# Kernel tuning notes

Measured on AMD Instinct MI355X. Metric: run time of the kernel, lower is better.

## Reference

```python
import jax, jax.numpy as jnp
import numpy as np

N_NODES = 50000
N_EDGES = 800000
FIN = 128
FQK = 128
FV = 128
H = 8


def setup_inputs() -> dict:
    key = jax.random.key(0)
    k1, k2, k3, k4, k5 = jax.random.split(key, 5)
    x = jax.random.normal(k1, (N_NODES, FIN), dtype=jnp.float32)
    # nn.Linear(Fin, 2*Fqk+Fv, bias=False): weight shape [Ftot, Fin]
    W = jax.random.normal(k2, (2 * FQK + FV, FIN), dtype=jnp.float32) / np.sqrt(FIN)
    # src must be sorted (scatter_* assume batch[-1]+1 segments)
    src = jnp.sort(jax.random.randint(k3, (N_EDGES,), 0, N_NODES))
    dest = jax.random.randint(k4, (N_EDGES,), 0, N_NODES)
    ei = jnp.stack([src, dest])
    batch = jnp.sort(jax.random.randint(k5, (N_NODES,), 0, 64))
    return {"x": x, "W": W, "batch": batch, "ei": ei}


def reference(x, W, batch, ei):
    n = x.shape[0]
    Fh = FQK // H    # 16
    Fhv = FV // H    # 16
    scaling = float(Fh) ** (-0.5)
    src, dest = ei[0], ei[1]

    qkv = x @ W.T                                   # [n, 2*Fqk+Fv]
    q = (qkv[:, :FQK] * scaling).reshape(n, H, Fh)
    k = qkv[:, FQK:2 * FQK].reshape(n, H, Fh)
    v = qkv[:, 2 * FQK:].reshape(n, H, Fhv)

    # per-edge attention scores, one per head: [E, H]
    aw = jnp.einsum('ehf,ehf->eh', q[src], k[dest])
    # faithful to original scatter_softmax: subtract GLOBAL per-head max
    aw = aw - aw.max(axis=0)
    ex = jnp.exp(aw)
    denom = jax.ops.segment_sum(ex, src, num_segments=n)[src]   # [E, H]
    a = ex / denom

    out = jax.ops.segment_sum(a[:, :, None] * v[dest], src, num_segments=n)  # [n, H, Fhv]
    return out.reshape(n, H * Fhv)
```

## Files before the change

kernel.cpp:

```cpp
#include <hip/hip_runtime.h>
#include <hip/hip_fp16.h>
#include <math.h>

#define FIN_ 128

typedef _Float16 half2v __attribute__((ext_vector_type(2)));
typedef _Float16 half8v __attribute__((ext_vector_type(8)));
typedef __attribute__((ext_vector_type(4))) float float4v;

__device__ __forceinline__ half2v u2h(unsigned u) {
    union { unsigned u; half2v h; } c; c.u = u; return c.h;
}

__device__ __forceinline__ half8v cvt8(float4 a, float4 b) {
    half8v r;
    r[0] = (_Float16)a.x; r[1] = (_Float16)a.y;
    r[2] = (_Float16)a.z; r[3] = (_Float16)a.w;
    r[4] = (_Float16)b.x; r[5] = (_Float16)b.y;
    r[6] = (_Float16)b.z; r[7] = (_Float16)b.w;
    return r;
}

__global__ __launch_bounds__(256) void gemm_qkv_mfma(const float* __restrict__ x,
                                                     const float* __restrict__ W,
                                                     _Float16* __restrict__ qb,
                                                     _Float16* __restrict__ kv,
                                                     int n) {
    __shared__ _Float16 smem[2 * 128 * 68];
    _Float16 (*xs)[68] = (_Float16(*)[68])smem;
    _Float16 (*ws)[68] = (_Float16(*)[68])(smem + 128 * 68);
    const int row0 = blockIdx.x * 128;
    const int f0   = blockIdx.y * 128;
    const int t = threadIdx.x;
    const int lane = t & 63;
    const int wave = t >> 6;
    const int wr = wave >> 1, wc = wave & 1;
    const int l15 = lane & 15, kg = lane >> 4;

    float4v acc[4][4];
#pragma unroll
    for (int i = 0; i < 4; ++i)
#pragma unroll
        for (int j = 0; j < 4; ++j) acc[i][j] = (float4v)0.f;

    const int r5 = t >> 3;
    const int c8 = (t & 7) * 8;

    for (int half = 0; half < 2; ++half) {
        __syncthreads();
#pragma unroll
        for (int p = 0; p < 4; ++p) {
            const int row = p * 32 + r5;
            const int gxr = row0 + row;
            float4 u0 = make_float4(0.f, 0.f, 0.f, 0.f), u1 = u0;
            if (gxr < n) {
                u0 = *(const float4*)&x[(size_t)gxr * FIN_ + half * 64 + c8];
                u1 = *(const float4*)&x[(size_t)gxr * FIN_ + half * 64 + c8 + 4];
            }
            *(half8v*)&xs[row][c8] = cvt8(u0, u1);
            const float4 w0 = *(const float4*)&W[(size_t)(f0 + row) * FIN_ + half * 64 + c8];
            const float4 w1 = *(const float4*)&W[(size_t)(f0 + row) * FIN_ + half * 64 + c8 + 4];
            *(half8v*)&ws[row][c8] = cvt8(w0, w1);
        }
        __syncthreads();
#pragma unroll
        for (int ks = 0; ks < 2; ++ks) {
            const int kcol = ks * 32 + kg * 8;
            half8v a[4], b[4];
#pragma unroll
            for (int mi = 0; mi < 4; ++mi)
                a[mi] = *(half8v*)&ws[wr * 64 + mi * 16 + l15][kcol];
#pragma unroll
            for (int ni = 0; ni < 4; ++ni)
                b[ni] = *(half8v*)&xs[wc * 64 + ni * 16 + l15][kcol];
#pragma unroll
            for (int mi = 0; mi < 4; ++mi)
#pragma unroll
                for (int ni = 0; ni < 4; ++ni)
                    acc[mi][ni] = __builtin_amdgcn_mfma_f32_16x16x32_f16(
                        a[mi], b[ni], acc[mi][ni], 0, 0, 0);
        }
    }

    __syncthreads();
    _Float16 (*T)[136] = (_Float16(*)[136])smem;
    const bool isq = (f0 == 0);
    const float s = isq ? 0.25f : 1.0f;
#pragma unroll
    for (int mi = 0; mi < 4; ++mi) {
        const int fb = wr * 64 + mi * 16 + kg * 4;
#pragma unroll
        for (int ni = 0; ni < 4; ++ni) {
            const int nl = wc * 64 + ni * 16 + l15;
            union { ushort4 u; _Float16 f[4]; } pk;
#pragma unroll
            for (int r = 0; r < 4; ++r) pk.f[r] = (_Float16)(acc[mi][ni][r] * s);
            *(ushort4*)&T[nl][fb] = pk.u;
        }
    }
    __syncthreads();
#pragma unroll
    for (int i = 0; i < 8; ++i) {
        const int u = t + i * 256;
        const int nl = u >> 4;
        const int cs = (u & 15) * 8;
        const int ng = row0 + nl;
        if (ng >= n) continue;
        const half8v val = *(const half8v*)&T[nl][cs];
        if (isq) *(half8v*)&qb[(size_t)ng * 128 + cs] = val;
        else     *(half8v*)&kv[(size_t)ng * 256 + (f0 - 128) + cs] = val;
    }
}

__global__ void build_rowptr(const int* __restrict__ src, int nE,
                             int* __restrict__ rowptr, int n) {
    int i = blockIdx.x * blockDim.x + threadIdx.x;
    if (i > n) return;
    int lo = 0, hi = nE;
    while (lo < hi) {
        int mid = (lo + hi) >> 1;
        if (src[mid] < i) lo = mid + 1; else hi = mid;
    }
    rowptr[i] = lo;
}

__device__ __forceinline__ float dot16(uint4 k0, uint4 k1, const half2v* q) {
#if __has_builtin(__builtin_amdgcn_fdot2)
    float s = __builtin_amdgcn_fdot2(u2h(k0.x), q[0], 0.f, false);
    s = __builtin_amdgcn_fdot2(u2h(k0.y), q[1], s, false);
    s = __builtin_amdgcn_fdot2(u2h(k0.z), q[2], s, false);
    s = __builtin_amdgcn_fdot2(u2h(k0.w), q[3], s, false);
    s = __builtin_amdgcn_fdot2(u2h(k1.x), q[4], s, false);
    s = __builtin_amdgcn_fdot2(u2h(k1.y), q[5], s, false);
    s = __builtin_amdgcn_fdot2(u2h(k1.z), q[6], s, false);
    s = __builtin_amdgcn_fdot2(u2h(k1.w), q[7], s, false);
    return s;
#else
    half2v a = u2h(k0.x) * q[0];
    a += u2h(k0.y) * q[1];
    a += u2h(k0.z) * q[2];
    a += u2h(k0.w) * q[3];
    a += u2h(k1.x) * q[4];
    a += u2h(k1.y) * q[5];
    a += u2h(k1.z) * q[6];
    a += u2h(k1.w) * q[7];
    return (float)a[0] + (float)a[1];
#endif
}

__global__ __launch_bounds__(256) void attn_edges_ep(const _Float16* __restrict__ qb,
                                                     const _Float16* __restrict__ kv,
                                                     const int* __restrict__ rowptr,
                                                     const int* __restrict__ dest,
                                                     float* __restrict__ out, int n) {
    const int wave = threadIdx.x >> 6;
    const int node = blockIdx.x * 4 + wave;
    if (node >= n) return;
    const int lane = threadIdx.x & 63;
    const int j = lane >> 3;
    const int h = lane & 7;
    const int ppos = ((j & 1) << 3) | ((j & 2) << 1) | ((j & 4) >> 1);
    float* outp = &out[(size_t)node * FIN_ + h * 16 + ppos];

    const int e0 = rowptr[node];
    const int e1 = rowptr[node + 1];
    if (e0 == e1) {
        *(float2*)outp = make_float2(0.f, 0.f);
        return;
    }

    half2v qh[8];
    {
        const uint4 q0 = *(const uint4*)(qb + (size_t)node * 128 + h * 16);
        const uint4 q1 = *(const uint4*)(qb + (size_t)node * 128 + h * 16 + 8);
        qh[0] = u2h(q0.x); qh[1] = u2h(q0.y); qh[2] = u2h(q0.z); qh[3] = u2h(q0.w);
        qh[4] = u2h(q1.x); qh[5] = u2h(q1.y); qh[6] = u2h(q1.z); qh[7] = u2h(q1.w);
    }

    float lsum = 0.f;
    half2v a8[8];
#pragma unroll
    for (int i = 0; i < 8; ++i) a8[i] = (half2v)(_Float16)0;

    const int hoff = h << 4;
    for (int eb = e0; eb < e1; eb += 16) {
        const int eA = eb + j;
        const int eB = eb + 8 + j;
        const bool vA = eA < e1;
        const bool vB = eB < e1;
        const unsigned dA = (unsigned)dest[vA ? eA : (e1 - 1)];
        const unsigned dB = (unsigned)dest[vB ? eB : (e1 - 1)];
        const unsigned offA = (dA << 8) + hoff;
        const unsigned offB = (dB << 8) + hoff;
        const uint4 k0A = *(const uint4*)(kv + offA);
        const uint4 k1A = *(const uint4*)(kv + offA + 8);
        const uint4 v0A = *(const uint4*)(kv + offA + 128);
        const uint4 v1A = *(const uint4*)(kv + offA + 136);
        const uint4 k0B = *(const uint4*)(kv + offB);
        const uint4 k1B = *(const uint4*)(kv + offB + 8);
        const uint4 v0B = *(const uint4*)(kv + offB + 128);
        const uint4 v1B = *(const uint4*)(kv + offB + 136);

        const float sA = dot16(k0A, k1A, qh);
        const float sB = dot16(k0B, k1B, qh);
        const float pA = vA ? __expf(sA) : 0.f;
        const float pB = vB ? __expf(sB) : 0.f;
        lsum += pA + pB;

        const _Float16 ha = (_Float16)pA, hb = (_Float16)pB;
        const half2v pa = {ha, ha}, pb = {hb, hb};
        a8[0] += pa * u2h(v0A.x) + pb * u2h(v0B.x);
        a8[1] += pa * u2h(v0A.y) + pb * u2h(v0B.y);
        a8[2] += pa * u2h(v0A.z) + pb * u2h(v0B.z);
        a8[3] += pa * u2h(v0A.w) + pb * u2h(v0B.w);
        a8[4] += pa * u2h(v1A.x) + pb * u2h(v1B.x);
        a8[5] += pa * u2h(v1A.y) + pb * u2h(v1B.y);
        a8[6] += pa * u2h(v1A.z) + pb * u2h(v1B.z);
        a8[7] += pa * u2h(v1A.w) + pb * u2h(v1B.w);
    }

    lsum += __shfl_xor(lsum, 8);
    lsum += __shfl_xor(lsum, 16);
    lsum += __shfl_xor(lsum, 32);

    float a16[16];
#pragma unroll
    for (int i = 0; i < 8; ++i) {
        a16[2 * i]     = (float)a8[i][0];
        a16[2 * i + 1] = (float)a8[i][1];
    }

    float r8[8];
    {
        const bool b = (j & 1) != 0;
#pragma unroll
        for (int i = 0; i < 8; ++i) {
            const float keep = b ? a16[i + 8] : a16[i];
            const float send = b ? a16[i] : a16[i + 8];
            r8[i] = keep + __shfl_xor(send, 8);
        }
    }
    float r4[4];
    {
        const bool b = (j & 2) != 0;
#pragma unroll
        for (int i = 0; i < 4; ++i) {
            const float keep = b ? r8[i + 4] : r8[i];
            const float send = b ? r8[i] : r8[i + 4];
            r4[i] = keep + __shfl_xor(send, 16);
        }
    }
    float r2[2];
    {
        const bool b = (j & 4) != 0;
#pragma unroll
        for (int i = 0; i < 2; ++i) {
            const float keep = b ? r4[i + 2] : r4[i];
            const float send = b ? r4[i] : r4[i + 2];
            r2[i] = keep + __shfl_xor(send, 32);
        }
    }

    const float inv = (lsum > 0.f) ? 1.f / lsum : 0.f;
    *(float2*)outp = make_float2(r2[0] * inv, r2[1] * inv);
}

extern "C" void kernel_launch(void* const* d_in, const int* in_sizes, int n_in,
                              void* d_out, int out_size, void* d_ws, size_t ws_size,
                              hipStream_t stream) {
    const float* x = (const float*)d_in[0];
    const float* W = (const float*)d_in[1];
    const int* ei = (const int*)d_in[3];

    const int n = in_sizes[0] / FIN_;
    const int nE = in_sizes[3] / 2;
    const int* src = ei;
    const int* dest = ei + nE;

    char* w = (char*)d_ws;
    _Float16* qb = (_Float16*)w;   w += (size_t)n * 128 * 2;
    _Float16* kv = (_Float16*)w;   w += (size_t)n * 256 * 2;
    int* rowptr = (int*)w;
    float* out = (float*)d_out;

    build_rowptr<<<(n + 1 + 255) / 256, 256, 0, stream>>>(src, nE, rowptr, n);

    dim3 g1((n + 127) / 128, 3);
    gemm_qkv_mfma<<<g1, 256, 0, stream>>>(x, W, qb, kv, n);

    attn_edges_ep<<<(n + 3) / 4, 256, 0, stream>>>(qb, kv, rowptr, dest, out, n);
}
```

Measured before the change: 99.74 us.

## Fuse rowptr build into QKV GEMM kernel and load MFMA operands directly from global

Merges the rowptr binary-search kernel and the QKV GEMM into one launch, using extra blocks for the rowptr work, which removes a kernel launch and its gap. The GEMM no longer stages x and W through shared memory. Each lane loads and converts its MFMA fragments straight from global memory, so the staging syncs go away at the cost of redundant, less coalesced global reads that rely on L2/L1. The three feature-block tiles for a row block are now adjacent in block order to improve x reuse in cache. The output transpose buffer is halved and written in two phases, which lowers LDS use and may raise occupancy.

```diff
diff --git a/kernel.cpp b/kernel.cpp
--- a/kernel.cpp
+++ b/kernel.cpp
@@ -3,6 +3,7 @@
 #include <math.h>
 
 #define FIN_ 128
+#define NGB_ 3
 
 typedef _Float16 half2v __attribute__((ext_vector_type(2)));
 typedef _Float16 half8v __attribute__((ext_vector_type(8)));
@@ -21,17 +22,32 @@
     return r;
 }
 
-__global__ __launch_bounds__(256) void gemm_qkv_mfma(const float* __restrict__ x,
-                                                     const float* __restrict__ W,
-                                                     _Float16* __restrict__ qb,
-                                                     _Float16* __restrict__ kv,
-                                                     int n) {
-    __shared__ _Float16 smem[2 * 128 * 68];
-    _Float16 (*xs)[68] = (_Float16(*)[68])smem;
-    _Float16 (*ws)[68] = (_Float16(*)[68])(smem + 128 * 68);
-    const int row0 = blockIdx.x * 128;
-    const int f0   = blockIdx.y * 128;
+__global__ __launch_bounds__(256) void prep_kernel(const float* __restrict__ x,
+                                                   const float* __restrict__ W,
+                                                   _Float16* __restrict__ qb,
+                                                   _Float16* __restrict__ kv,
+                                                   const int* __restrict__ src,
+                                                   int* __restrict__ rowptr,
+                                                   int n, int nE, int nxb) {
+    const int bid = blockIdx.x;
     const int t = threadIdx.x;
+
+    if (bid >= 3 * nxb) {
+        const int i = (bid - 3 * nxb) * 256 + t;
+        if (i > n) return;
+        int lo = 0, hi = nE;
+        while (lo < hi) {
+            int mid = (lo + hi) >> 1;
+            if (src[mid] < i) lo = mid + 1; else hi = mid;
+        }
+        rowptr[i] = lo;
+        return;
+    }
+
+    __shared__ _Float16 T[64][136];
+    const int bx = bid / 3, fsel = bid % 3;
+    const int row0 = bx * 128;
+    const int f0 = fsel * 128;
     const int lane = t & 63;
     const int wave = t >> 6;
     const int wr = wave >> 1, wc = wave & 1;
@@ -43,36 +59,30 @@
 #pragma unroll
         for (int j = 0; j < 4; ++j) acc[i][j] = (float4v)0.f;
 
-    const int r5 = t >> 3;
-    const int c8 = (t & 7) * 8;
-
+    int nodeIdx[4];
+#pragma unroll
+    for (int ni = 0; ni < 4; ++ni) {
+        const int nd = row0 + wc * 64 + ni * 16 + l15;
+        nodeIdx[ni] = (nd < n) ? nd : 0;
+    }
+    const size_t fbase = (size_t)(f0 + wr * 64 + l15) * FIN_;
+
+#pragma unroll
     for (int half = 0; half < 2; ++half) {
-        __syncthreads();
-#pragma unroll
-        for (int p = 0; p < 4; ++p) {
-            const int row = p * 32 + r5;
-            const int gxr = row0 + row;
-            float4 u0 = make_float4(0.f, 0.f, 0.f, 0.f), u1 = u0;
-            if (gxr < n) {
-                u0 = *(const float4*)&x[(size_t)gxr * FIN_ + half * 64 + c8];
-                u1 = *(const float4*)&x[(size_t)gxr * FIN_ + half * 64 + c8 + 4];
-            }
-            *(half8v*)&xs[row][c8] = cvt8(u0, u1);
-            const float4 w0 = *(const float4*)&W[(size_t)(f0 + row) * FIN_ + half * 64 + c8];
-            const float4 w1 = *(const float4*)&W[(size_t)(f0 + row) * FIN_ + half * 64 + c8 + 4];
-            *(half8v*)&ws[row][c8] = cvt8(w0, w1);
-        }
-        __syncthreads();
 #pragma unroll
         for (int ks = 0; ks < 2; ++ks) {
-            const int kcol = ks * 32 + kg * 8;
+            const int koff = half * 64 + ks * 32 + kg * 8;
             half8v a[4], b[4];
 #pragma unroll
-            for (int mi = 0; mi < 4; ++mi)
-                a[mi] = *(half8v*)&ws[wr * 64 + mi * 16 + l15][kcol];
-#pragma unroll
-            for (int ni = 0; ni < 4; ++ni)
-                b[ni] = *(half8v*)&xs[wc * 64 + ni * 16 + l15][kcol];
+            for (int mi = 0; mi < 4; ++mi) {
+                const float* p = W + fbase + (size_t)mi * 16 * FIN_ + koff;
+                a[mi] = cvt8(*(const float4*)p, *(const float4*)(p + 4));
+            }
+#pragma unroll
+            for (int ni = 0; ni < 4; ++ni) {
+                const float* p = x + (size_t)nodeIdx[ni] * FIN_ + koff;
+                b[ni] = cvt8(*(const float4*)p, *(const float4*)(p + 4));
+            }
 #pragma unroll
             for (int mi = 0; mi < 4; ++mi)
 #pragma unroll
@@ -82,46 +92,38 @@
         }
     }
 
-    __syncthreads();
-    _Float16 (*T)[136] = (_Float16(*)[136])smem;
-    const bool isq = (f0 == 0);
+    const bool isq = (fsel == 0);
     const float s = isq ? 0.25f : 1.0f;
-#pragma unroll
-    for (int mi = 0; mi < 4; ++mi) {
-        const int fb = wr * 64 + mi * 16 + kg * 4;
-#pragma unroll
-        for (int ni = 0; ni < 4; ++ni) {
-            const int nl = wc * 64 + ni * 16 + l15;
-            union { ushort4 u; _Float16 f[4]; } pk;
-#pragma unroll
-            for (int r = 0; r < 4; ++r) pk.f[r] = (_Float16)(acc[mi][ni][r] * s);
-            *(ushort4*)&T[nl][fb] = pk.u;
-        }
-    }
-    __syncthreads();
-#pragma unroll
-    for (int i = 0; i < 8; ++i) {
-        const int u = t + i * 256;
-        const int nl = u >> 4;
-        const int cs = (u & 15) * 8;
-        const int ng = row0 + nl;
-        if (ng >= n) continue;
-        const half8v val = *(const half8v*)&T[nl][cs];
-        if (isq) *(half8v*)&qb[(size_t)ng * 128 + cs] = val;
-        else     *(half8v*)&kv[(size_t)ng * 256 + (f0 - 128) + cs] = val;
-    }
-}
-
-__global__ void build_rowptr(const int* __restrict__ src, int nE,
-                             int* __restrict__ rowptr, int n) {
-    int i = blockIdx.x * blockDim.x + threadIdx.x;
-    if (i > n) return;
-    int lo = 0, hi = nE;
-    while (lo < hi) {
-        int mid = (lo + hi) >> 1;
-        if (src[mid] < i) lo = mid + 1; else hi = mid;
-    }
-    rowptr[i] = lo;
+    for (int ph = 0; ph < 2; ++ph) {
+        if (wc == ph) {
+#pragma unroll
+            for (int mi = 0; mi < 4; ++mi) {
+                const int fb = wr * 64 + mi * 16 + kg * 4;
+#pragma unroll
+                for (int ni = 0; ni < 4; ++ni) {
+                    const int nl = ni * 16 + l15;
+                    union { ushort4 u; _Float16 f[4]; } pk;
+#pragma unroll
+                    for (int r = 0; r < 4; ++r) pk.f[r] = (_Float16)(acc[mi][ni][r] * s);
+                    *(ushort4*)&T[nl][fb] = pk.u;
+                }
+            }
+        }
+        __syncthreads();
+#pragma unroll
+        for (int i = 0; i < 4; ++i) {
+            const int u = t + i * 256;
+            const int nl = u >> 4;
+            const int cs = (u & 15) * 8;
+            const int ng = row0 + ph * 64 + nl;
+            if (ng < n) {
+                const half8v val = *(const half8v*)&T[nl][cs];
+                if (isq) *(half8v*)&qb[(size_t)ng * 128 + cs] = val;
+                else     *(half8v*)&kv[(size_t)ng * 256 + (f0 - 128) + cs] = val;
+            }
+        }
+        __syncthreads();
+    }
 }
 
 __device__ __forceinline__ float dot16(uint4 k0, uint4 k1, const half2v* q) {
@@ -283,10 +285,9 @@
     int* rowptr = (int*)w;
     float* out = (float*)d_out;
 
-    build_rowptr<<<(n + 1 + 255) / 256, 256, 0, stream>>>(src, nE, rowptr, n);
-
-    dim3 g1((n + 127) / 128, 3);
-    gemm_qkv_mfma<<<g1, 256, 0, stream>>>(x, W, qb, kv, n);
+    const int nxb = (n + 127) / 128;
+    const int nrb = (n + 1 + 255) / 256;
+    prep_kernel<<<3 * nxb + nrb, 256, 0, stream>>>(x, W, qb, kv, src, rowptr, n, nE, nxb);
 
     attn_edges_ep<<<(n + 3) / 4, 256, 0, stream>>>(qb, kv, rowptr, dest, out, n);
 }
```

New measurement: 104.9 us. 1.05x slower.
